# Kernel tuning notes

Measured on AMD Instinct MI355X. Metric: run time of the kernel, lower is better.

The kernel has to match this reference:

```python
import jax, jax.numpy as jnp
import numpy as np

MO = 48          # max_output_len (positional slots)
D = 32           # d_inner
NA = 8           # n_actions
STOP = 0
CAT_PRIM, CAT_MOD, CAT_COMB = 0, 1, 2


def _mlp(feats, w1, b1, w2, b2, w3, b3):
    # Linear -> GELU(exact, erf) -> Linear -> GELU -> Linear (torch nn.GELU default is exact)
    h = jax.nn.gelu(feats @ w1.T + b1, approximate=False)
    h = jax.nn.gelu(h @ w2.T + b2, approximate=False)
    return h @ w3.T + b3


def setup_inputs() -> dict:
    key = jax.random.key(0)
    ks = jax.random.split(key, 20)
    B, N = 1024, 16
    inp = {
        'node_cats': jax.random.randint(ks[0], (B, N), 0, 3, dtype=jnp.int32),
        'node_subs': jax.random.randint(ks[1], (B, N), 0, 2, dtype=jnp.int32),
        'node_mask': jax.random.randint(ks[2], (B, N), 0, 2, dtype=jnp.int32),
        'child_left': jax.random.randint(ks[3], (B, N), 0, N, dtype=jnp.int32),
        'child_right': jax.random.randint(ks[4], (B, N), 0, N, dtype=jnp.int32),
        'action_embed': jax.random.normal(ks[5], (NA, D), jnp.float32),
        'mod_w1': jax.random.normal(ks[6], (128, 3), jnp.float32) * 0.1,
        'mod_b1': jax.random.normal(ks[7], (128,), jnp.float32) * 0.02,
        'mod_w2': jax.random.normal(ks[8], (128, 128), jnp.float32) * 0.05,
        'mod_b2': jax.random.normal(ks[9], (128,), jnp.float32) * 0.02,
        'mod_w3': jax.random.normal(ks[10], (MO * MO, 128), jnp.float32) * 0.01,
        'mod_b3': (4.0 * jnp.eye(MO)).flatten(),  # identity-ish init as in torch code
        'comb_w1': jax.random.normal(ks[11], (128, 4), jnp.float32) * 0.1,
        'comb_b1': jax.random.normal(ks[12], (128,), jnp.float32) * 0.02,
        'comb_w2': jax.random.normal(ks[13], (128, 128), jnp.float32) * 0.05,
        'comb_b2': jax.random.normal(ks[14], (128,), jnp.float32) * 0.02,
        'comb_w3': jax.random.normal(ks[15], (MO * 2 * MO, 128), jnp.float32) * 0.01,
        'comb_b3': (4.0 * jnp.eye(MO, 2 * MO)).flatten(),
    }
    return inp


def _forward(node_cats, node_subs, node_mask, child_left, child_right,
             action_embed, mod_w1, mod_b1, mod_w2, mod_b2, mod_w3, mod_b3,
             comb_w1, comb_b1, comb_w2, comb_b2, comb_w3, comb_b3):
    B, N = node_cats.shape
    mask = node_mask.astype(bool)
    cl = jnp.clip(child_left, 0, N - 1)
    cr = jnp.clip(child_right, 0, N - 1)
    prim_mask = (node_cats == CAT_PRIM) & mask
    mod_mask = (node_cats == CAT_MOD) & mask
    comb_mask = (node_cats == CAT_COMB) & mask
    subs01 = jnp.clip(node_subs, 0, 1)
    sub_oh = jax.nn.one_hot(subs01, 2, dtype=jnp.float32)  # (B,N,2)

    # --- primitive init: buffer[0] = action_embed[subs+1], zeros elsewhere ---
    action_ids = jnp.clip(node_subs + 1, 0, NA - 1)
    prim_vecs = action_embed[action_ids]  # (B,N,D)
    buffers = jnp.zeros((B, N, MO, D), jnp.float32)
    buffers = buffers.at[:, :, 0, :].set(prim_vecs * prim_mask[..., None].astype(jnp.float32))
    counts = prim_mask.astype(jnp.float32)  # (B,N)

    # --- modifier stage ---
    child_buf = jnp.take_along_axis(buffers, cl[:, :, None, None], axis=1)  # (B,N,MO,D)
    child_cnt = jnp.take_along_axis(counts, cl, axis=1)  # (B,N)
    feats = jnp.concatenate([child_cnt[..., None] / MO, sub_oh], axis=-1)  # (B,N,3)
    logits = _mlp(feats, mod_w1, mod_b1, mod_w2, mod_b2, mod_w3, mod_b3).reshape(B, N, MO, MO)
    attn = jax.nn.softmax(logits, axis=-1)
    mod_buf = jnp.einsum('bnpq,bnqd->bnpd', attn, child_buf)
    factors = jnp.array([2.0, 3.0], jnp.float32)[subs01]
    mod_cnt = jnp.minimum(child_cnt * factors, float(MO))
    buffers = jnp.where(mod_mask[:, :, None, None], mod_buf, buffers)
    counts = jnp.where(mod_mask, mod_cnt, counts)

    # --- combinator stage ---
    left_buf = jnp.take_along_axis(buffers, cl[:, :, None, None], axis=1)
    right_buf = jnp.take_along_axis(buffers, cr[:, :, None, None], axis=1)
    left_cnt = jnp.take_along_axis(counts, cl, axis=1)
    right_cnt = jnp.take_along_axis(counts, cr, axis=1)
    feats = jnp.concatenate([left_cnt[..., None] / MO, right_cnt[..., None] / MO, sub_oh], axis=-1)  # (B,N,4)
    logits = _mlp(feats, comb_w1, comb_b1, comb_w2, comb_b2, comb_w3, comb_b3).reshape(B, N, MO, 2 * MO)
    attn = jax.nn.softmax(logits, axis=-1)
    concat_buf = jnp.concatenate([left_buf, right_buf], axis=2)  # (B,N,2MO,D)
    comb_buf = jnp.einsum('bnpq,bnqd->bnpd', attn, concat_buf)
    comb_cnt = jnp.minimum(left_cnt + right_cnt, float(MO))
    buffers = jnp.where(comb_mask[:, :, None, None], comb_buf, buffers)
    counts = jnp.where(comb_mask, comb_cnt, counts)

    # --- decode root with tied embedding + stop bias ---
    root_buf = buffers[:, 0, :, :]  # (B,MO,D)
    out = jnp.einsum('bpd,ad->bpa', root_buf, action_embed)  # (B,MO,NA)
    positions = jnp.arange(MO, dtype=jnp.float32)[None, :]  # (1,MO)
    is_stop = (positions >= counts[:, 0:1]).astype(jnp.float32)[..., None]  # (B,MO,1)
    stop_bias = jnp.zeros((NA,), jnp.float32).at[STOP].set(8.0)
    return out + is_stop * stop_bias


def reference(node_cats, node_subs, node_mask, child_left, child_right,
              action_embed, mod_w1, mod_b1, mod_w2, mod_b2, mod_w3, mod_b3,
              comb_w1, comb_b1, comb_w2, comb_b2, comb_w3, comb_b3):
    return _forward(node_cats, node_subs, node_mask, child_left, child_right,
                    action_embed, mod_w1, mod_b1, mod_w2, mod_b2, mod_w3, mod_b3,
                    comb_w1, comb_b1, comb_w2, comb_b2, comb_w3, comb_b3)
```

## Files before the change

kernel.cpp:

```cpp
#include <hip/hip_runtime.h>
#include <hip/hip_bf16.h>
#include <float.h>


#define NNODE 16

#define MODCOL_OFF 0
#define C0_OFF     192
#define C48_OFF    1728
#define DOTL_OFF   3264
#define DOTR_OFF   9408
#define G_OFF      15552
#define H2_OFF     15616

__device__ __forceinline__ float gelu_exact(float x) {
    return 0.5f * x * (1.0f + erff(x * 0.70710678118654752f));
}

__device__ __forceinline__ float dot128(const float* __restrict__ w,
                                        const float* __restrict__ h) {
    const float4* w4 = (const float4*)w;
    float s = 0.f;
    #pragma unroll
    for (int i = 0; i < 32; ++i) {
        float4 v = w4[i];
        s += v.x * h[4 * i + 0] + v.y * h[4 * i + 1] +
             v.z * h[4 * i + 2] + v.w * h[4 * i + 3];
    }
    return s;
}

__global__ __launch_bounds__(128) void scan_tables_a(
    const float* __restrict__ E,
    const float* __restrict__ mw1, const float* __restrict__ mb1,
    const float* __restrict__ mw2, const float* __restrict__ mb2,
    const float* __restrict__ mw3, const float* __restrict__ mb3,
    const float* __restrict__ cw1, const float* __restrict__ cb1,
    const float* __restrict__ cw2, const float* __restrict__ cb2,
    float* __restrict__ ws)
{
    __shared__ float h1[128];
    __shared__ float h2s[128];
    __shared__ float lg[48];

    const int tid = threadIdx.x;
    const int blk = blockIdx.x;

    if (blk < 192) {
        const int m = blk / 48, p = blk % 48;
        const int cnt = m >> 1, sub = m & 1;
        const float f0 = (float)cnt / 48.0f;
        const float f1 = (sub == 0) ? 1.0f : 0.0f;
        const float f2 = (sub == 1) ? 1.0f : 0.0f;
        h1[tid] = gelu_exact(mw1[tid * 3 + 0] * f0 + mw1[tid * 3 + 1] * f1 +
                             mw1[tid * 3 + 2] * f2 + mb1[tid]);
        __syncthreads();
        h2s[tid] = gelu_exact(dot128(mw2 + tid * 128, h1) + mb2[tid]);
        __syncthreads();
        if (tid < 48)
            lg[tid] = dot128(mw3 + (p * 48 + tid) * 128, h2s) + mb3[p * 48 + tid];
        __syncthreads();
        if (tid == 0) {
            float mx = lg[0];
            for (int q = 1; q < 48; ++q) mx = fmaxf(mx, lg[q]);
            float s = 0.f;
            for (int q = 0; q < 48; ++q) s += expf(lg[q] - mx);
            ws[MODCOL_OFF + m * 48 + p] = expf(lg[0] - mx) / s;
        }
        return;
    }
    if (blk < 224) {
        const int c = blk - 192;
        const int csub = c & 1;
        const int rc = (c >> 1) & 3;
        const int lc = (c >> 3) & 3;
        const float f0 = (float)lc / 48.0f;
        const float f1 = (float)rc / 48.0f;
        const float f2 = (csub == 0) ? 1.0f : 0.0f;
        const float f3 = (csub == 1) ? 1.0f : 0.0f;
        h1[tid] = gelu_exact(cw1[tid * 4 + 0] * f0 + cw1[tid * 4 + 1] * f1 +
                             cw1[tid * 4 + 2] * f2 + cw1[tid * 4 + 3] * f3 + cb1[tid]);
        __syncthreads();
        ws[H2_OFF + c * 128 + tid] =
            gelu_exact(dot128(cw2 + tid * 128, h1) + cb2[tid]);
        return;
    }
    if (tid < 64) {
        const int i = tid >> 3, a = tid & 7;
        float s = 0.f;
        #pragma unroll
        for (int d = 0; d < 32; ++d) s += E[i * 32 + d] * E[a * 32 + d];
        ws[G_OFF + tid] = s;
    }
}

__global__ __launch_bounds__(128) void scan_tables_b(
    const float* __restrict__ cw3, const float* __restrict__ cb3,
    float* __restrict__ ws)
{
    __shared__ float h2s[128];
    __shared__ float pr[96];
    __shared__ float mc[192];
    __shared__ float red[128];

    const int tid = threadIdx.x;
    const int c = blockIdx.x / 48;
    const int p = blockIdx.x % 48;

    h2s[tid] = ws[H2_OFF + c * 128 + tid];
    if (tid < 64) mc[tid] = ws[MODCOL_OFF + tid];
    else if (tid < 128 && tid >= 64) { if (tid - 64 < 128) mc[64 + (tid - 64)] = ws[MODCOL_OFF + 64 + (tid - 64)]; }
    if (tid < 64) mc[128 + tid] = ws[MODCOL_OFF + 128 + tid];
    __syncthreads();

    float lv = -FLT_MAX;
    if (tid < 96)
        lv = dot128(cw3 + (p * 96 + tid) * 128, h2s) + cb3[p * 96 + tid];

    red[tid] = lv;
    __syncthreads();
    for (int s = 64; s > 0; s >>= 1) {
        if (tid < s) red[tid] = fmaxf(red[tid], red[tid + s]);
        __syncthreads();
    }
    const float mx = red[0];
    __syncthreads();

    float ev = (tid < 96) ? expf(lv - mx) : 0.f;
    if (tid < 96) pr[tid] = ev;
    red[tid] = ev;
    __syncthreads();
    for (int s = 64; s > 0; s >>= 1) {
        if (tid < s) red[tid] += red[tid + s];
        __syncthreads();
    }
    const float inv = 1.0f / red[0];

    if (tid == 0) {
        ws[C0_OFF + c * 48 + p]  = pr[0]  * inv;
        ws[C48_OFF + c * 48 + p] = pr[48] * inv;
    }
    if (tid < 8) {
        const int m = tid & 3;
        const int side = tid >> 2;
        const float* q0 = pr + side * 48;
        float s = 0.f;
        #pragma unroll
        for (int q = 0; q < 48; ++q) s += q0[q] * mc[m * 48 + q];
        const int off = (side == 0 ? DOTL_OFF : DOTR_OFF) + (c * 4 + m) * 48 + p;
        ws[off] = s * inv;
    }
}

__global__ __launch_bounds__(384) void scan_output(
    const int* __restrict__ cats, const int* __restrict__ subs,
    const int* __restrict__ mask, const int* __restrict__ cl,
    const int* __restrict__ cr,
    const float* __restrict__ ws,
    float* __restrict__ out)
{
    __shared__ int sc[NNODE], ss[NNODE], sm[NNODE], sl[NNODE], sr[NNODE];
    __shared__ int s_dec[7];
    __shared__ float s_G[64];

    const int b = blockIdx.x;
    const int tid = threadIdx.x;
    if (tid < NNODE) {
        sc[tid] = cats[b * NNODE + tid];
        ss[tid] = subs[b * NNODE + tid];
        sm[tid] = mask[b * NNODE + tid];
        sl[tid] = cl[b * NNODE + tid];
        sr[tid] = cr[b * NNODE + tid];
    } else if (tid >= 64 && tid < 128) {
        s_G[tid - 64] = ws[G_OFF + tid - 64];
    }
    __syncthreads();

    if (tid == 0) {
        auto clampN  = [](int x) { return x < 0 ? 0 : (x > NNODE - 1 ? NNODE - 1 : x); };
        auto clamp01 = [](int x) { return x < 0 ? 0 : (x > 1 ? 1 : x); };
        auto clampA  = [](int x) { return x < 0 ? 0 : (x > 7 ? 7 : x); };
        auto PRIM = [&](int n) { return (sc[n] == 0) && (sm[n] != 0); };
        auto MODM = [&](int n) { return (sc[n] == 1) && (sm[n] != 0); };
        auto AID  = [&](int n) { return clampA(ss[n] + 1); };

        int modeL = 0, modeR = 0, offL = 0, offR = 0, aidL = 0, aidR = 0, count0 = 0;
        const int  cat0 = sc[0];
        const bool msk0 = sm[0] != 0;
        const int  sub0 = clamp01(ss[0]);
        const int  cl0  = clampN(sl[0]);
        const int  cr0  = clampN(sr[0]);

        if (cat0 == 2 && msk0) {
            auto cnt2 = [&](int n) -> int {
                if (MODM(n)) {
                    int c1 = PRIM(clampN(sl[n])) ? 1 : 0;
                    int f  = clamp01(ss[n]) ? 3 : 2;
                    int v  = c1 * f;
                    return v > 48 ? 48 : v;
                }
                return PRIM(n) ? 1 : 0;
            };
            const int l = cl0, r = cr0;
            const int lcc = cnt2(l), rcc = cnt2(r);
            const int cidx = (lcc * 4 + rcc) * 2 + sub0;
            count0 = lcc + rcc; if (count0 > 48) count0 = 48;
            if (MODM(l)) {
                const int g = clampN(sl[l]);
                if (PRIM(g)) {
                    modeL = 1; aidL = AID(g);
                    const int mcfg = 2 + clamp01(ss[l]);
                    offL = DOTL_OFF + (cidx * 4 + mcfg) * 48;
                }
            } else if (PRIM(l)) {
                modeL = 1; aidL = AID(l);
                offL = C0_OFF + cidx * 48;
            }
            if (MODM(r)) {
                const int g = clampN(sl[r]);
                if (PRIM(g)) {
                    modeR = 1; aidR = AID(g);
                    const int mcfg = 2 + clamp01(ss[r]);
                    offR = DOTR_OFF + (cidx * 4 + mcfg) * 48;
                }
            } else if (PRIM(r)) {
                modeR = 1; aidR = AID(r);
                offR = C48_OFF + cidx * 48;
            }
        } else if (cat0 == 1 && msk0) {
            const int ch = cl0;
            const int c1 = PRIM(ch) ? 1 : 0;
            count0 = c1 * (sub0 ? 3 : 2); if (count0 > 48) count0 = 48;
            if (c1) {
                modeL = 1; aidL = AID(ch);
                offL = MODCOL_OFF + (2 + sub0) * 48;
            }
        } else if (cat0 == 0 && msk0) {
            modeL = 2; aidL = AID(0); count0 = 1;
        }
        s_dec[0] = modeL; s_dec[1] = modeR; s_dec[2] = offL; s_dec[3] = offR;
        s_dec[4] = aidL;  s_dec[5] = aidR;  s_dec[6] = count0;
    }
    __syncthreads();

    const int p = tid >> 3, a = tid & 7;
    const int modeL = s_dec[0], modeR = s_dec[1];
    float v = 0.f;
    if (modeL == 1)       v += ws[s_dec[2] + p] * s_G[s_dec[4] * 8 + a];
    else if (modeL == 2)  { if (p == 0) v = s_G[s_dec[4] * 8 + a]; }
    if (modeR == 1)       v += ws[s_dec[3] + p] * s_G[s_dec[5] * 8 + a];
    if (a == 0 && p >= s_dec[6]) v += 8.0f;
    out[b * 384 + tid] = v;
}

extern "C" void kernel_launch(void* const* d_in, const int* in_sizes, int n_in,
                              void* d_out, int out_size, void* d_ws, size_t ws_size,
                              hipStream_t stream) {
    const int* cats = (const int*)d_in[0];
    const int* subs = (const int*)d_in[1];
    const int* mask = (const int*)d_in[2];
    const int* cl   = (const int*)d_in[3];
    const int* cr   = (const int*)d_in[4];
    const float* E   = (const float*)d_in[5];
    const float* mw1 = (const float*)d_in[6];
    const float* mb1 = (const float*)d_in[7];
    const float* mw2 = (const float*)d_in[8];
    const float* mb2 = (const float*)d_in[9];
    const float* mw3 = (const float*)d_in[10];
    const float* mb3 = (const float*)d_in[11];
    const float* cw1 = (const float*)d_in[12];
    const float* cb1 = (const float*)d_in[13];
    const float* cw2 = (const float*)d_in[14];
    const float* cb2 = (const float*)d_in[15];
    const float* cw3 = (const float*)d_in[16];
    const float* cb3 = (const float*)d_in[17];
    float* ws  = (float*)d_ws;
    float* out = (float*)d_out;
    const int B = in_sizes[0] / NNODE;

    scan_tables_a<<<225, 128, 0, stream>>>(E, mw1, mb1, mw2, mb2, mw3, mb3,
                                           cw1, cb1, cw2, cb2, ws);
    scan_tables_b<<<32 * 48, 128, 0, stream>>>(cw3, cb3, ws);
    scan_output<<<B, 384, 0, stream>>>(cats, subs, mask, cl, cr, ws, out);
}
```

Before: 111.1 us.

## Coalesce comb_w3 GEMV loads and use wave-shuffle softmax reductions in scan_tables_b

Rewrites scan_tables_b so that four lanes cooperate on each weight row. Each lane loads interleaved float4 chunks and the partial sums are combined with shuffles, so the reads of cw3 are coalesced instead of each thread striding through its own row. The softmax max and sum reductions now use wave-level shuffle reductions in place of shared-memory tree loops with many barriers. Block indexing is remapped so that blocks adjacent in launch order share the same p rows of cw3 across different c values, which may improve cache reuse of the weight rows. A launch-bounds occupancy hint is also added.

```diff
diff --git a/kernel.cpp b/kernel.cpp
--- a/kernel.cpp
+++ b/kernel.cpp
@@ -94,60 +94,76 @@
     }
 }
 
-__global__ __launch_bounds__(128) void scan_tables_b(
+__global__ __launch_bounds__(128, 4) void scan_tables_b(
     const float* __restrict__ cw3, const float* __restrict__ cb3,
     float* __restrict__ ws)
 {
     __shared__ float h2s[128];
+    __shared__ float mc[192];
+    __shared__ float lg[96];
     __shared__ float pr[96];
-    __shared__ float mc[192];
-    __shared__ float red[128];
+    __shared__ float red[4];
 
     const int tid = threadIdx.x;
-    const int c = blockIdx.x / 48;
-    const int p = blockIdx.x % 48;
+    const int p = blockIdx.x >> 5;
+    const int c = blockIdx.x & 31;
 
     h2s[tid] = ws[H2_OFF + c * 128 + tid];
-    if (tid < 64) mc[tid] = ws[MODCOL_OFF + tid];
-    else if (tid < 128 && tid >= 64) { if (tid - 64 < 128) mc[64 + (tid - 64)] = ws[MODCOL_OFF + 64 + (tid - 64)]; }
-    if (tid < 64) mc[128 + tid] = ws[MODCOL_OFF + 128 + tid];
-    __syncthreads();
-
-    float lv = -FLT_MAX;
-    if (tid < 96)
-        lv = dot128(cw3 + (p * 96 + tid) * 128, h2s) + cb3[p * 96 + tid];
-
-    red[tid] = lv;
-    __syncthreads();
-    for (int s = 64; s > 0; s >>= 1) {
-        if (tid < s) red[tid] = fmaxf(red[tid], red[tid + s]);
-        __syncthreads();
-    }
-    const float mx = red[0];
-    __syncthreads();
+    for (int i = tid; i < 192; i += 128) mc[i] = ws[MODCOL_OFF + i];
+    __syncthreads();
+
+    const int j = tid & 3;
+    const int rbase = tid >> 2;
+    const float4* h24 = (const float4*)h2s;
+    #pragma unroll
+    for (int o = 0; o < 3; ++o) {
+        const int r = o * 32 + rbase;
+        const float4* w4 = (const float4*)(cw3 + (p * 96 + r) * 128);
+        float s = 0.f;
+        #pragma unroll
+        for (int i = 0; i < 8; ++i) {
+            const int f4i = i * 4 + j;
+            float4 w = w4[f4i];
+            float4 h = h24[f4i];
+            s += w.x * h.x + w.y * h.y + w.z * h.z + w.w * h.w;
+        }
+        s += __shfl_xor(s, 1);
+        s += __shfl_xor(s, 2);
+        if (j == 0) lg[r] = s;
+    }
+    __syncthreads();
+
+    const int wv = tid >> 6;
+    float lv = (tid < 96) ? (lg[tid] + cb3[p * 96 + tid]) : -FLT_MAX;
+    float m = lv;
+    #pragma unroll
+    for (int d = 32; d > 0; d >>= 1) m = fmaxf(m, __shfl_xor(m, d));
+    if ((tid & 63) == 0) red[wv] = m;
+    __syncthreads();
+    const float mx = fmaxf(red[0], red[1]);
 
     float ev = (tid < 96) ? expf(lv - mx) : 0.f;
     if (tid < 96) pr[tid] = ev;
-    red[tid] = ev;
-    __syncthreads();
-    for (int s = 64; s > 0; s >>= 1) {
-        if (tid < s) red[tid] += red[tid + s];
-        __syncthreads();
-    }
-    const float inv = 1.0f / red[0];
+    float sum = ev;
+    #pragma unroll
+    for (int d = 32; d > 0; d >>= 1) sum += __shfl_xor(sum, d);
+    if ((tid & 63) == 0) red[2 + wv] = sum;
+    __syncthreads();
+    const float inv = 1.0f / (red[2] + red[3]);
 
     if (tid == 0) {
         ws[C0_OFF + c * 48 + p]  = pr[0]  * inv;
         ws[C48_OFF + c * 48 + p] = pr[48] * inv;
     }
     if (tid < 8) {
-        const int m = tid & 3;
+        const int mm = tid & 3;
         const int side = tid >> 2;
         const float* q0 = pr + side * 48;
+        const float* mr = mc + mm * 48;
         float s = 0.f;
         #pragma unroll
-        for (int q = 0; q < 48; ++q) s += q0[q] * mc[m * 48 + q];
-        const int off = (side == 0 ? DOTL_OFF : DOTR_OFF) + (c * 4 + m) * 48 + p;
+        for (int q = 0; q < 48; ++q) s += q0[q] * mr[q];
+        const int off = (side == 0 ? DOTL_OFF : DOTR_OFF) + (c * 4 + mm) * 48 + p;
         ws[off] = s * inv;
     }
 }
@@ -280,6 +296,6 @@
 
     scan_tables_a<<<225, 128, 0, stream>>>(E, mw1, mb1, mw2, mb2, mw3, mb3,
                                            cw1, cb1, cw2, cb2, ws);
-    scan_tables_b<<<32 * 48, 128, 0, stream>>>(cw3, cb3, ws);
+    scan_tables_b<<<48 * 32, 128, 0, stream>>>(cw3, cb3, ws);
     scan_output<<<B, 384, 0, stream>>>(cats, subs, mask, cl, cr, ws, out);
 }
```

Result: faster. 107.5 us (-3.2%).
